# Kernel optimization log

Measured on AMD Instinct MI355X. Metric: run time of the kernel, lower is better.

The kernel has to match this reference:

```python
import jax, jax.numpy as jnp
import numpy as np

B, C, E, HLR, WLR = 2, 64, 4, 192, 192


def setup_inputs() -> dict:
    key = jax.random.key(0)
    ks = jax.random.split(key, 8)
    s = 0.05  # keep activations/offsets in a sane range
    return {
        "x": jax.random.normal(ks[0], (B, C, HLR, WLR), jnp.float32),
        "fused": jax.random.normal(ks[1], (B, C, HLR, WLR), jnp.float32),
        "weight_compress": jax.random.normal(ks[2], (E, C // 8, C), jnp.float32) * s,
        "weight_expand": jax.random.normal(ks[3], (E, C, C // 8), jnp.float32) * s,
        "body_w1": jax.random.normal(ks[4], (64, 4), jnp.float32) * s,
        "body_b1": jnp.zeros((64,), jnp.float32),
        "body_w2": jax.random.normal(ks[5], (64, 64), jnp.float32) * s,
        "body_b2": jnp.zeros((64,), jnp.float32),
        "routing_w": jax.random.normal(ks[6], (E, 64), jnp.float32) * s,
        "routing_b": jnp.zeros((E,), jnp.float32),
        "offset_w": jax.random.normal(ks[7], (2, 64), jnp.float32) * s,
        "offset_b": jnp.zeros((2,), jnp.float32),
        "scale": 2,
    }


def _conv1x1(x, w, b):
    # x: [n, cin, H, W], w: [cout, cin] (1x1 conv)
    return jnp.einsum('oc,nchw->nohw', w, x) + b[None, :, None, None]


def _grid_sample(img, px, py):
    # Bilinear sample, align_corners=True semantics, zeros padding.
    # img: [b,c,h,w]; px, py: [b,H,W] absolute LR pixel coords.
    b, c, h, w = img.shape
    x0 = jnp.floor(px)
    y0 = jnp.floor(py)
    wx = (px - x0)[:, None]  # [b,1,H,W]
    wy = (py - y0)[:, None]

    def gather(xi, yi):
        valid = (xi >= 0) & (xi <= w - 1) & (yi >= 0) & (yi <= h - 1)
        xc = jnp.clip(xi, 0, w - 1).astype(jnp.int32)
        yc = jnp.clip(yi, 0, h - 1).astype(jnp.int32)
        v = jax.vmap(lambda im, yy, xx: im[:, yy, xx])(img, yc, xc)  # [b,c,H,W]
        return v * valid[:, None].astype(img.dtype)

    v00 = gather(x0, y0)
    v01 = gather(x0 + 1, y0)
    v10 = gather(x0, y0 + 1)
    v11 = gather(x0 + 1, y0 + 1)
    top = v00 * (1 - wx) + v01 * wx
    bot = v10 * (1 - wx) + v11 * wx
    return top * (1 - wy) + bot * wy


def reference(x, fused, weight_compress, weight_expand, body_w1, body_b1,
              body_w2, body_b2, routing_w, routing_b, offset_w, offset_b, scale):
    b, c, h, w = fused.shape
    H, W = round(h * scale), round(w * scale)
    e, c8 = weight_compress.shape[0], weight_compress.shape[1]

    ch = jnp.arange(H, dtype=jnp.float32)
    cw = jnp.arange(W, dtype=jnp.float32)
    coor_h = (ch + 0.5) / scale - jnp.floor((ch + 0.5) / scale + 0.001) - 0.5  # [H]
    coor_w = (cw + 0.5) / scale - jnp.floor((cw + 0.5) / scale + 0.001) - 0.5  # [W]
    inp = jnp.stack([
        jnp.full((H, W), 1.0 / scale, jnp.float32),
        jnp.full((H, W), 1.0 / scale, jnp.float32),
        jnp.broadcast_to(coor_h[:, None], (H, W)),
        jnp.broadcast_to(coor_w[None, :], (H, W)),
    ], 0)[None]  # [1,4,H,W]

    emb = jax.nn.relu(_conv1x1(inp, body_w1, body_b1))
    emb = jax.nn.relu(_conv1x1(emb, body_w2, body_b2))
    offset = _conv1x1(emb, offset_w, offset_b)            # [1,2,H,W]
    routing = jax.nn.sigmoid(_conv1x1(emb, routing_w, routing_b))  # [1,E,H,W]

    rw = routing.reshape(e, H * W).T                      # [HW, E]
    wc = (rw @ weight_compress.reshape(e, -1)).reshape(H, W, c8, c)  # per-pixel compress
    we = (rw @ weight_expand.reshape(e, -1)).reshape(H, W, c, c8)    # per-pixel expand

    # deformable sample: HR grid projected into LR space + learned offset (pixel units)
    px = jnp.broadcast_to((cw[None, :] + 0.5) / scale - 0.5, (H, W))[None] + offset[:, 0]
    py = jnp.broadcast_to((ch[:, None] + 0.5) / scale - 0.5, (H, W))[None] + offset[:, 1]
    px = jnp.broadcast_to(px, (b, H, W))
    py = jnp.broadcast_to(py, (b, H, W))
    fea0 = _grid_sample(fused, px, py)                    # [b,c,H,W]

    fea = fea0.transpose(0, 2, 3, 1)                      # [b,H,W,c]
    mid = jnp.einsum('hwoc,bhwc->bhwo', wc, fea)          # [b,H,W,c//8]
    out = jnp.einsum('hwco,bhwo->bhwc', we, mid)          # [b,H,W,c]
    return out.transpose(0, 3, 1, 2) + fea0
```

## Files before the change

kernel.cpp:

```cpp
#include <hip/hip_runtime.h>
#include <hip/hip_bf16.h>
#include <math.h>

typedef __attribute__((ext_vector_type(8))) short short8;
typedef __attribute__((ext_vector_type(4))) float f32x4;

#define HLR_ 192
#define WLR_ 192
#define H_ 384
#define W_ 384
#define LRP (HLR_*WLR_)
#define PTILES (LRP/64)
#define TPX 128
#define NTW (W_/TPX)

#define WS_K_OFF 4718592
#define WS_OFF_OFF (WS_K_OFF + 8192)

__device__ __forceinline__ unsigned short f32_bf16(float x){
    union { float f; unsigned int u; } v; v.f = x;
    unsigned int r = v.u + 0x7fffu + ((v.u >> 16) & 1u);
    return (unsigned short)(r >> 16);
}
__device__ __forceinline__ unsigned int pk_bf16(float a, float b){
    float2 t; t.x = a; t.y = b;
    __hip_bfloat162 h = __float22bfloat162_rn(t);
    union { __hip_bfloat162 h; unsigned int u; } c; c.h = h;
    return c.u;
}

__global__ __launch_bounds__(256) void prep_kernel(
    const float* __restrict__ fused, float* __restrict__ fused_t,
    const float* __restrict__ w1, const float* __restrict__ b1,
    const float* __restrict__ w2, const float* __restrict__ b2,
    const float* __restrict__ rw, const float* __restrict__ rb,
    const float* __restrict__ ow, const float* __restrict__ ob,
    const float* __restrict__ WC, const float* __restrict__ WE,
    unsigned short* __restrict__ Kmat, float* __restrict__ g_off)
{
    __shared__ float smem[8912];
    int bid = blockIdx.x;
    int tid = threadIdx.x;

    if (bid == 0) {
        float* sW2 = smem;
        float* sRW = smem + 4160;
        float* sE1 = smem + 4544;
        float* sR  = smem + 4800;
        float* sWc = smem + 4816;
        float* sWe = smem + 6864;

        for (int idx = tid; idx < 4096; idx += 256)
            sW2[(idx>>6)*65 + (idx&63)] = w2[idx];
        sRW[tid] = rw[tid];
        if (tid < 128) sRW[256 + tid] = ow[tid];

        int wave = tid >> 6, lane = tid & 63;
        int ph = wave >> 1, pw = wave & 1;

        float ch = (ph + 0.5f)*0.5f;
        float coor_h = ch - floorf(ch + 0.001f) - 0.5f;
        float cw = (pw + 0.5f)*0.5f;
        float coor_w = cw - floorf(cw + 0.001f) - 0.5f;

        float e1 = w1[lane*4+0]*0.5f + w1[lane*4+1]*0.5f
                 + w1[lane*4+2]*coor_h + w1[lane*4+3]*coor_w + b1[lane];
        sE1[wave*64 + lane] = fmaxf(e1, 0.0f);
        __syncthreads();

        float e2 = b2[lane];
        #pragma unroll 16
        for (int i = 0; i < 64; ++i) e2 += sW2[lane*65 + i] * sE1[wave*64 + i];
        e2 = fmaxf(e2, 0.0f);

        #pragma unroll
        for (int k = 0; k < 6; ++k) {
            float t = sRW[k*64 + lane] * e2;
            #pragma unroll
            for (int m = 1; m <= 32; m <<= 1) t += __shfl_xor(t, m, 64);
            if (lane == 0) {
                if (k < 4) sR[wave*4 + k] = 1.0f/(1.0f + expf(-(t + rb[k])));
                else       g_off[wave*2 + (k-4)] = t + ob[k-4];
            }
        }
        __syncthreads();

        for (int idx = tid; idx < 2048; idx += 256) {
            int cls = idx >> 9, rem = idx & 511;
            float r0=sR[cls*4+0], r1=sR[cls*4+1], r2=sR[cls*4+2], r3=sR[cls*4+3];
            sWc[cls*512 + rem] =
                r0*WC[0*512+rem] + r1*WC[1*512+rem] + r2*WC[2*512+rem] + r3*WC[3*512+rem];
        }
        for (int idx = tid; idx < 2048; idx += 256) {
            int cls = idx >> 9, rem = idx & 511;
            float r0=sR[cls*4+0], r1=sR[cls*4+1], r2=sR[cls*4+2], r3=sR[cls*4+3];
            sWe[cls*512 + rem] =
                r0*WE[0*512+rem] + r1*WE[1*512+rem] + r2*WE[2*512+rem] + r3*WE[3*512+rem];
        }
        __syncthreads();

        for (int idx = tid; idx < 16384; idx += 256) {
            int cls = idx >> 12, rem = idx & 4095;
            int c = rem >> 6, cp = rem & 63;
            float a = (c == cp) ? 1.0f : 0.0f;
            #pragma unroll
            for (int o = 0; o < 8; ++o)
                a += sWe[cls*512 + c*8 + o] * sWc[cls*512 + o*64 + cp];
            Kmat[idx] = f32_bf16(a);
        }
    } else {
        float* tile = smem;
        int id = bid - 1;
        int b = id / PTILES, pt = id % PTILES;
        int p0 = pt * 64;
        int tlo = tid & 63, thi = tid >> 6;
        #pragma unroll
        for (int i = 0; i < 16; ++i) {
            int c = thi + i*4;
            tile[c*65 + tlo] = fused[(size_t)(b*64 + c)*LRP + p0 + tlo];
        }
        __syncthreads();
        #pragma unroll
        for (int i = 0; i < 16; ++i) {
            int p = thi + i*4;
            fused_t[(size_t)(b*LRP + p0 + p)*64 + tlo] = tile[tlo*65 + p];
        }
    }
}

__global__ __launch_bounds__(256, 4) void main_kernel(
    const float* __restrict__ fused_t, const unsigned short* __restrict__ Kmat,
    const float* __restrict__ g_off, float* __restrict__ out)
{
    __shared__ unsigned short sFea[256*72];

    int g = blockIdx.x;
    int xcd = g & 7;
    int t = g >> 3;
    int q = t / 3;
    int wt = t - q*3;
    int h = xcd*48 + q;
    int w0 = wt * TPX;
    int tid = threadIdx.x, wave = tid >> 6, lane = tid & 63;
    int b = wave >> 1, par = wave & 1;
    int ph = h & 1, cls = ph*2 + par;

    float off0 = g_off[cls*2 + 0];
    float off1 = g_off[cls*2 + 1];

    float py  = (h + 0.5f)*0.5f - 0.5f + off1;
    float y0f = floorf(py);
    float wy  = py - y0f;
    int   y0  = (int)y0f;
    float fy0 = (y0 >= 0  && y0 <= HLR_-1) ? 1.0f : 0.0f;
    float fy1 = (y0 >= -1 && y0 <= HLR_-2) ? 1.0f : 0.0f;
    int   yc0 = min(max(y0, 0), HLR_-1);
    int   yc1 = min(max(y0+1, 0), HLR_-1);
    float omwy = 1.0f - wy;

    float pxb  = (w0 + par + 0.5f)*0.5f - 0.5f + off0;
    float x0bf = floorf(pxb);
    float wx   = pxb - x0bf;
    int   x0b  = (int)x0bf;
    float omwx = 1.0f - wx;

    float W00 = omwx*omwy*fy0, W01 = wx*omwy*fy0;
    float W10 = omwx*wy  *fy1, W11 = wx*wy  *fy1;

    int itg = lane >> 4;
    int cg  = lane & 15;

    const float* baseB = fused_t + (size_t)b * LRP * 64;
    const float* r0 = baseB + (size_t)yc0 * WLR_ * 64 + cg*4;
    const float* r1 = baseB + (size_t)yc1 * WLR_ * 64 + cg*4;
    unsigned short* sW = sFea + wave*64*72 + cg*4;

    #pragma unroll
    for (int j = 0; j < 16; ++j) {
        int item = j*4 + itg;
        int x0 = x0b + item;
        float fx0 = (x0 >= 0  && x0 <= WLR_-1) ? 1.0f : 0.0f;
        float fx1 = (x0 >= -1 && x0 <= WLR_-2) ? 1.0f : 0.0f;
        int xc0 = min(max(x0, 0), WLR_-1);
        int xc1 = min(max(x0+1, 0), WLR_-1);
        float a00 = W00*fx0, a01 = W01*fx1, a10 = W10*fx0, a11 = W11*fx1;
        f32x4 v00 = *(const f32x4*)(r0 + (size_t)xc0*64);
        f32x4 v01 = *(const f32x4*)(r0 + (size_t)xc1*64);
        f32x4 v10 = *(const f32x4*)(r1 + (size_t)xc0*64);
        f32x4 v11 = *(const f32x4*)(r1 + (size_t)xc1*64);
        f32x4 v = v00*a00 + v01*a01 + v10*a10 + v11*a11;
        uint2 pv;
        pv.x = pk_bf16(v[0], v[1]);
        pv.y = pk_bf16(v[2], v[3]);
        *(uint2*)(sW + item*72) = pv;
    }
    __syncthreads();

    int lm = lane & 15, lg = lane >> 4;

    short8 Bf[2][4];
    #pragma unroll
    for (int nt = 0; nt < 4; ++nt)
        #pragma unroll
        for (int kt = 0; kt < 2; ++kt)
            Bf[kt][nt] = *(const short8*)(sFea + (wave*64 + nt*16 + lm)*72 + kt*32 + lg*8);

    const unsigned short* Kc = Kmat + cls*4096;
    short8 Af[4][2];
    #pragma unroll
    for (int mt = 0; mt < 4; ++mt)
        #pragma unroll
        for (int kt = 0; kt < 2; ++kt)
            Af[mt][kt] = *(const short8*)(Kc + (mt*16 + lm)*64 + kt*32 + lg*8);

    f32x4 acc[4][4];
    #pragma unroll
    for (int mt = 0; mt < 4; ++mt) {
        #pragma unroll
        for (int nt = 0; nt < 4; ++nt) {
            f32x4 a = {0.0f, 0.0f, 0.0f, 0.0f};
            a = __builtin_amdgcn_mfma_f32_16x16x32_bf16(Af[mt][0], Bf[0][nt], a, 0, 0, 0);
            a = __builtin_amdgcn_mfma_f32_16x16x32_bf16(Af[mt][1], Bf[1][nt], a, 0, 0, 0);
            acc[mt][nt] = a;
        }
    }

    #pragma unroll
    for (int mt = 0; mt < 4; ++mt) {
        #pragma unroll
        for (int nt = 0; nt < 4; ++nt) {
            int wc = w0 + 2*(nt*16 + lm) + par;
            int c0 = mt*16 + lg*4;
            float* op = out + (((size_t)(b*64 + c0)*H_ + h)*W_ + wc);
            op[0*(size_t)(H_*W_)] = acc[mt][nt][0];
            op[1*(size_t)(H_*W_)] = acc[mt][nt][1];
            op[2*(size_t)(H_*W_)] = acc[mt][nt][2];
            op[3*(size_t)(H_*W_)] = acc[mt][nt][3];
        }
    }
}

extern "C" void kernel_launch(void* const* d_in, const int* in_sizes, int n_in,
                              void* d_out, int out_size, void* d_ws, size_t ws_size,
                              hipStream_t stream)
{
    const float* fused = (const float*)d_in[1];
    const float* WC    = (const float*)d_in[2];
    const float* WE    = (const float*)d_in[3];
    const float* w1    = (const float*)d_in[4];
    const float* b1    = (const float*)d_in[5];
    const float* w2    = (const float*)d_in[6];
    const float* b2    = (const float*)d_in[7];
    const float* rw    = (const float*)d_in[8];
    const float* rb    = (const float*)d_in[9];
    const float* ow    = (const float*)d_in[10];
    const float* ob    = (const float*)d_in[11];
    (void)in_sizes; (void)n_in; (void)out_size; (void)ws_size;

    float* ws = (float*)d_ws;
    float* fused_t = ws;
    unsigned short* Kmat = (unsigned short*)(ws + WS_K_OFF);
    float* g_off = ws + WS_OFF_OFF;
    float* o = (float*)d_out;

    hipLaunchKernelGGL(prep_kernel, dim3(1 + 2*PTILES), dim3(256), 0, stream,
                       fused, fused_t, w1, b1, w2, b2, rw, rb, ow, ob, WC, WE,
                       Kmat, g_off);
    hipLaunchKernelGGL(main_kernel, dim3(H_*NTW), dim3(256), 0, stream,
                       fused_t, Kmat, g_off, o);
}
```

Before: 150.5 us.

## Shrink pixel tile, reuse sliding bilinear taps, swizzle LDS, raise occupancy

```diff
diff --git a/kernel.cpp b/kernel.cpp
--- a/kernel.cpp
+++ b/kernel.cpp
@@ -11,8 +11,9 @@
 #define W_ 384
 #define LRP (HLR_*WLR_)
 #define PTILES (LRP/64)
-#define TPX 128
+#define TPX 96
 #define NTW (W_/TPX)
+#define IPW 48
 
 #define WS_K_OFF 4718592
 #define WS_OFF_OFF (WS_K_OFF + 8192)
@@ -128,17 +129,17 @@
     }
 }
 
-__global__ __launch_bounds__(256, 4) void main_kernel(
+__global__ __launch_bounds__(256, 6) void main_kernel(
     const float* __restrict__ fused_t, const unsigned short* __restrict__ Kmat,
     const float* __restrict__ g_off, float* __restrict__ out)
 {
-    __shared__ unsigned short sFea[256*72];
+    __shared__ unsigned short sFea[4*IPW*64];
 
     int g = blockIdx.x;
     int xcd = g & 7;
     int t = g >> 3;
-    int q = t / 3;
-    int wt = t - q*3;
+    int q = t >> 2;
+    int wt = t & 3;
     int h = xcd*48 + q;
     int w0 = wt * TPX;
     int tid = threadIdx.x, wave = tid >> 6, lane = tid & 63;
@@ -173,37 +174,34 @@
     const float* baseB = fused_t + (size_t)b * LRP * 64;
     const float* r0 = baseB + (size_t)yc0 * WLR_ * 64 + cg*4;
     const float* r1 = baseB + (size_t)yc1 * WLR_ * 64 + cg*4;
-    unsigned short* sW = sFea + wave*64*72 + cg*4;
+    unsigned short* sBaseW = sFea + ((wave*IPW) << 6) + (((cg & 1) << 2));
+    int wchunk = cg >> 1;
+
+    int xs = x0b + itg*12;
+    int xc = min(max(xs, 0), WLR_-1);
+    f32x4 p0 = *(const f32x4*)(r0 + (size_t)xc*64);
+    f32x4 p1 = *(const f32x4*)(r1 + (size_t)xc*64);
+    float fxp = (xs >= 0 && xs <= WLR_-1) ? 1.0f : 0.0f;
 
     #pragma unroll
-    for (int j = 0; j < 16; ++j) {
-        int item = j*4 + itg;
-        int x0 = x0b + item;
-        float fx0 = (x0 >= 0  && x0 <= WLR_-1) ? 1.0f : 0.0f;
-        float fx1 = (x0 >= -1 && x0 <= WLR_-2) ? 1.0f : 0.0f;
-        int xc0 = min(max(x0, 0), WLR_-1);
-        int xc1 = min(max(x0+1, 0), WLR_-1);
-        float a00 = W00*fx0, a01 = W01*fx1, a10 = W10*fx0, a11 = W11*fx1;
-        f32x4 v00 = *(const f32x4*)(r0 + (size_t)xc0*64);
-        f32x4 v01 = *(const f32x4*)(r0 + (size_t)xc1*64);
-        f32x4 v10 = *(const f32x4*)(r1 + (size_t)xc0*64);
-        f32x4 v11 = *(const f32x4*)(r1 + (size_t)xc1*64);
-        f32x4 v = v00*a00 + v01*a01 + v10*a10 + v11*a11;
+    for (int j = 0; j < 12; ++j) {
+        int xn = xs + j + 1;
+        float fxn = (xn >= 0 && xn <= WLR_-1) ? 1.0f : 0.0f;
+        int xcn = min(max(xn, 0), WLR_-1);
+        f32x4 c0 = *(const f32x4*)(r0 + (size_t)xcn*64);
+        f32x4 c1 = *(const f32x4*)(r1 + (size_t)xcn*64);
+        float a00 = W00*fxp, a01 = W01*fxn, a10 = W10*fxp, a11 = W11*fxn;
+        f32x4 v = p0*a00 + c0*a01 + p1*a10 + c1*a11;
         uint2 pv;
         pv.x = pk_bf16(v[0], v[1]);
         pv.y = pk_bf16(v[2], v[3]);
-        *(uint2*)(sW + item*72) = pv;
+        int item = itg*12 + j;
+        *(uint2*)(sBaseW + (item << 6) + (((wchunk ^ (item & 7)) << 3))) = pv;
+        p0 = c0; p1 = c1; fxp = fxn;
     }
     __syncthreads();
 
     int lm = lane & 15, lg = lane >> 4;
-
-    short8 Bf[2][4];
-    #pragma unroll
-    for (int nt = 0; nt < 4; ++nt)
-        #pragma unroll
-        for (int kt = 0; kt < 2; ++kt)
-            Bf[kt][nt] = *(const short8*)(sFea + (wave*64 + nt*16 + lm)*72 + kt*32 + lg*8);
 
     const unsigned short* Kc = Kmat + cls*4096;
     short8 Af[4][2];
@@ -213,29 +211,25 @@
         for (int kt = 0; kt < 2; ++kt)
             Af[mt][kt] = *(const short8*)(Kc + (mt*16 + lm)*64 + kt*32 + lg*8);
 
-    f32x4 acc[4][4];
     #pragma unroll
-    for (int mt = 0; mt < 4; ++mt) {
-        #pragma unroll
-        for (int nt = 0; nt < 4; ++nt) {
+    for (int nt = 0; nt < 3; ++nt) {
+        int slot = nt*16 + lm;
+        const unsigned short* sb = sFea + ((wave*IPW + slot) << 6);
+        short8 B0 = *(const short8*)(sb + (((0*4 + lg) ^ (slot & 7)) << 3));
+        short8 B1 = *(const short8*)(sb + (((1*4 + lg) ^ (slot & 7)) << 3));
+
+        int wc = w0 + 2*slot + par;
+        #pragma unroll
+        for (int mt = 0; mt < 4; ++mt) {
             f32x4 a = {0.0f, 0.0f, 0.0f, 0.0f};
-            a = __builtin_amdgcn_mfma_f32_16x16x32_bf16(Af[mt][0], Bf[0][nt], a, 0, 0, 0);
-            a = __builtin_amdgcn_mfma_f32_16x16x32_bf16(Af[mt][1], Bf[1][nt], a, 0, 0, 0);
-            acc[mt][nt] = a;
-        }
-    }
-
-    #pragma unroll
-    for (int mt = 0; mt < 4; ++mt) {
-        #pragma unroll
-        for (int nt = 0; nt < 4; ++nt) {
-            int wc = w0 + 2*(nt*16 + lm) + par;
+            a = __builtin_amdgcn_mfma_f32_16x16x32_bf16(Af[mt][0], B0, a, 0, 0, 0);
+            a = __builtin_amdgcn_mfma_f32_16x16x32_bf16(Af[mt][1], B1, a, 0, 0, 0);
             int c0 = mt*16 + lg*4;
             float* op = out + (((size_t)(b*64 + c0)*H_ + h)*W_ + wc);
-            op[0*(size_t)(H_*W_)] = acc[mt][nt][0];
-            op[1*(size_t)(H_*W_)] = acc[mt][nt][1];
-            op[2*(size_t)(H_*W_)] = acc[mt][nt][2];
-            op[3*(size_t)(H_*W_)] = acc[mt][nt][3];
+            op[0*(size_t)(H_*W_)] = a[0];
+            op[1*(size_t)(H_*W_)] = a[1];
+            op[2*(size_t)(H_*W_)] = a[2];
+            op[3*(size_t)(H_*W_)] = a[3];
         }
     }
 }
```

Result: no change. 149.0 us (-1.0%).
